# Kernel tuning notes

Hardware: AMD Instinct MI355X
Metric: run time of the kernel (lower is better)

## Reference

```python
import jax, jax.numpy as jnp
import numpy as np

B, Q, D, N = 128, 20, 11, 100000  # batch, produced vectors per sample, feature dim, song DB size
EPS = 1e-8  # torch cosine_similarity eps


def setup_inputs() -> dict:
    key = jax.random.key(0)
    ks = jax.random.split(key, 8)
    x = jax.random.normal(ks[0], (B, 5, 11), dtype=jnp.float32)
    W1 = jax.random.normal(ks[1], (55, 128), dtype=jnp.float32) * 0.1
    b1 = jnp.zeros((128,), dtype=jnp.float32)
    W2 = jax.random.normal(ks[2], (128, 64), dtype=jnp.float32) * 0.1
    b2 = jnp.zeros((64,), dtype=jnp.float32)
    W3 = jax.random.normal(ks[3], (64, Q * D), dtype=jnp.float32) * 0.1
    b3 = jnp.zeros((Q * D,), dtype=jnp.float32)
    songs = jax.random.normal(ks[4], (N, D), dtype=jnp.float32)
    return {"x": x, "W1": W1, "b1": b1, "W2": W2, "b2": b2, "W3": W3, "b3": b3, "songs": songs}


def reference(x, W1, b1, W2, b2, W3, b3, songs):
    # Encoder MLP: Flatten -> Linear -> ReLU -> Linear -> ReLU -> Linear
    h = x.reshape(x.shape[0], -1)                 # [B, 55]
    h = jax.nn.relu(h @ W1 + b1)                  # [B, 128]
    h = jax.nn.relu(h @ W2 + b2)                  # [B, 64]
    produced = (h @ W3 + b3).reshape(-1, Q, D)    # [B, 20, 11]

    # Batched cosine-similarity kNN (k=1 / argmax) against the song DB.
    # torch cosine_similarity: a.b / (max(||a||, eps) * max(||b||, eps))
    p_norm = produced / jnp.maximum(jnp.linalg.norm(produced, axis=-1, keepdims=True), EPS)
    s_norm = songs / jnp.maximum(jnp.linalg.norm(songs, axis=-1, keepdims=True), EPS)
    sim = jnp.einsum('bqd,nd->bqn', p_norm, s_norm)  # [B, Q, N]
    best = jnp.argmax(sim, axis=-1)                  # [B, Q]
    return songs[best]                                # [B, Q, D]
```

## Files before the change

kernel.cpp:

```cpp
#include <hip/hip_runtime.h>
#include <math.h>

#define EPS 1e-8f

constexpr int B_ = 128;
constexpr int Q_ = 20;
constexpr int D_ = 11;
constexpr int N_ = 100000;
constexpr int DP_ = 12;
constexpr int NPAIR = B_ * Q_;
constexpr int NCH = 2500;
constexpr int CS = N_ / NCH;
constexpr int NG = CS / 4;
constexpr int TPB = 128;
constexpr int PPT = 4;
constexpr int REP = NPAIR / (PPT * TPB);
constexpr int CPB = 2;
constexpr int NPB = NCH / CPB;
constexpr int MPAD = (NPB + 7) / 8;
constexpr int SGRID = 8 * MPAD * REP;

typedef __attribute__((ext_vector_type(4))) float f4;

__global__ void prep_kernel(const float* __restrict__ x,
                            const float* __restrict__ W1, const float* __restrict__ b1,
                            const float* __restrict__ W2, const float* __restrict__ b2,
                            const float* __restrict__ W3, const float* __restrict__ b3,
                            const float* __restrict__ songs,
                            float* __restrict__ pnorm, float* __restrict__ snorm,
                            int do_snorm)
{
    const int t = threadIdx.x;
    if (blockIdx.x >= B_) {
        if (!do_snorm) return;
        const int i = (blockIdx.x - B_) * blockDim.x + t;
        if (i >= N_) return;
        float v[DP_]; float ss = 0.0f;
#pragma unroll
        for (int d = 0; d < D_; ++d) { v[d] = songs[(size_t)i * D_ + d]; ss += v[d] * v[d]; }
        float nrm = fmaxf(sqrtf(ss), EPS);
#pragma unroll
        for (int d = 0; d < D_; ++d) v[d] /= nrm;
        v[D_] = 0.0f;
        float4* o = reinterpret_cast<float4*>(snorm + (size_t)i * DP_);
        o[0] = make_float4(v[0], v[1], v[2], v[3]);
        o[1] = make_float4(v[4], v[5], v[6], v[7]);
        o[2] = make_float4(v[8], v[9], v[10], v[11]);
        return;
    }
    __shared__ float xr[55];
    __shared__ float h1[128];
    __shared__ float h2[64];
    __shared__ float prod[220];
    const int b = blockIdx.x;
    if (t < 55) xr[t] = x[b * 55 + t];
    __syncthreads();
    if (t < 128) {
        float s = b1[t];
        for (int k = 0; k < 55; ++k) s += xr[k] * W1[k * 128 + t];
        h1[t] = fmaxf(s, 0.0f);
    }
    __syncthreads();
    if (t < 64) {
        float s = b2[t];
        for (int k = 0; k < 128; ++k) s += h1[k] * W2[k * 64 + t];
        h2[t] = fmaxf(s, 0.0f);
    }
    __syncthreads();
    if (t < 220) {
        float s = b3[t];
        for (int k = 0; k < 64; ++k) s += h2[k] * W3[k * 220 + t];
        prod[t] = s;
    }
    __syncthreads();
    if (t < Q_) {
        float ss = 0.0f;
        for (int d = 0; d < D_; ++d) { float v = prod[t * D_ + d]; ss += v * v; }
        float nrm = fmaxf(sqrtf(ss), EPS);
        float* o = pnorm + (b * Q_ + t) * DP_;
        for (int d = 0; d < D_; ++d) o[d] = prod[t * D_ + d] / nrm;
        o[D_] = 0.0f;
    }
}

__device__ __forceinline__ float dot11v(f4 qa, f4 qb, f4 qc,
                                        float4 a, float4 b, float4 c)
{
    float x = qa.x * a.x;
    x = fmaf(qa.y, a.y, x);
    x = fmaf(qa.z, a.z, x);
    x = fmaf(qa.w, a.w, x);
    x = fmaf(qb.x, b.x, x);
    x = fmaf(qb.y, b.y, x);
    x = fmaf(qb.z, b.z, x);
    x = fmaf(qb.w, b.w, x);
    x = fmaf(qc.x, c.x, x);
    x = fmaf(qc.y, c.y, x);
    x = fmaf(qc.z, c.z, x);
    return x;
}

__device__ __forceinline__ unsigned int fkey(float f)
{
    unsigned int b = __float_as_uint(f);
    return (b & 0x80000000u) ? ~b : (b | 0x80000000u);
}

__device__ __forceinline__ unsigned long long pack_vi(float v, int idx)
{
    return ((unsigned long long)fkey(v) << 32) | (unsigned long long)(0xFFFFFFFFu - (unsigned int)idx);
}

#define QLOAD(P, PTR) \
    asm volatile("global_load_dwordx4 %0, %3, off\n\t" \
                 "global_load_dwordx4 %1, %3, off offset:16\n\t" \
                 "global_load_dwordx4 %2, %3, off offset:32" \
                 : "=&v"(q##P##a), "=&v"(q##P##b), "=&v"(q##P##c) \
                 : "v"(PTR) : "memory")

#define QWAIT() \
    asm volatile("s_waitcnt vmcnt(0)" \
                 : "+v"(qAa), "+v"(qAb), "+v"(qAc), "+v"(qBa), "+v"(qBb), "+v"(qBc), \
                   "+v"(qCa), "+v"(qCb), "+v"(qCc), "+v"(qDa), "+v"(qDb), "+v"(qDc) \
                 :: "memory")

#define PMAXV(P, GCUR) { \
    float d0 = dot11v(q##P##a, q##P##b, q##P##c, s0, s1,  s2);  \
    float d1 = dot11v(q##P##a, q##P##b, q##P##c, s3, s4,  s5);  \
    float d2 = dot11v(q##P##a, q##P##b, q##P##c, s6, s7,  s8);  \
    float d3 = dot11v(q##P##a, q##P##b, q##P##c, s9, s10, s11); \
    float mx = fmaxf(fmaxf(d0, d1), fmaxf(d2, d3)); \
    if (mx > bv##P) { bv##P = mx; gi##P = (GCUR); } \
}

#define GSTEP(L4, GIDX, GOFF) { \
    const float4* vg = (L4) + (GIDX) * 12; \
    float4 s0 = vg[0], s1 = vg[1], s2  = vg[2],  s3  = vg[3],  s4  = vg[4],  s5  = vg[5]; \
    float4 s6 = vg[6], s7 = vg[7], s8  = vg[8],  s9  = vg[9],  s10 = vg[10], s11 = vg[11]; \
    PMAXV(A, (GOFF) + (GIDX)) PMAXV(B, (GOFF) + (GIDX)) \
    PMAXV(C, (GOFF) + (GIDX)) PMAXV(D, (GOFF) + (GIDX)) \
}

#define FINI(P, POFF) { \
    int gsel = gi##P; \
    int cs = (gsel >= NG) ? 1 : 0; \
    int gg = gsel - cs * NG; \
    const float4* vg = reinterpret_cast<const float4*>(lds[cs]) + gg * 12; \
    float4 s0 = vg[0], s1 = vg[1], s2  = vg[2],  s3  = vg[3],  s4  = vg[4],  s5  = vg[5]; \
    float4 s6 = vg[6], s7 = vg[7], s8  = vg[8],  s9  = vg[9],  s10 = vg[10], s11 = vg[11]; \
    float d0 = dot11v(q##P##a, q##P##b, q##P##c, s0, s1,  s2);  \
    float d1 = dot11v(q##P##a, q##P##b, q##P##c, s3, s4,  s5);  \
    float d2 = dot11v(q##P##a, q##P##b, q##P##c, s6, s7,  s8);  \
    float d3 = dot11v(q##P##a, q##P##b, q##P##c, s9, s10, s11); \
    int base = (c0 + cs) * CS + gg * 4; \
    int idx = base; \
    if (d3 == bv##P) idx = base + 3; \
    if (d2 == bv##P) idx = base + 2; \
    if (d1 == bv##P) idx = base + 1; \
    if (d0 == bv##P) idx = base; \
    atomicMax(&res[jb + (POFF) * TPB], pack_vi(bv##P, idx)); \
}

__global__ __launch_bounds__(TPB, 2)
void sim17_kernel(const float* __restrict__ pnorm,
                  const float* __restrict__ snorm,
                  unsigned long long* __restrict__ res)
{
    __shared__ __align__(16) float lds[CPB][CS * DP_];
    const int bid = blockIdx.x;
    const int u = bid & 7;
    const int kk = bid >> 3;
    const int r = kk % REP;
    const int m = kk / REP;
    const int cpair = u + 8 * m;
    if (cpair >= NPB) return;
    const int t = threadIdx.x;
    const int c0 = cpair * CPB;

    const float4* s40 = reinterpret_cast<const float4*>(snorm) + (size_t)c0 * CS * 3;
    const float4* s41 = s40 + CS * 3;
    float4* b0 = reinterpret_cast<float4*>(lds[0]);
    float4* b1 = reinterpret_cast<float4*>(lds[1]);

    if (t < CS * 3) b0[t] = s40[t];

    const int jb = r * (PPT * TPB) + t;
    f4 qAa, qAb, qAc, qBa, qBb, qBc, qCa, qCb, qCc, qDa, qDb, qDc;
    {
        const float* qp0 = pnorm + (size_t)(jb + 0 * TPB) * DP_;
        const float* qp1 = pnorm + (size_t)(jb + 1 * TPB) * DP_;
        const float* qp2 = pnorm + (size_t)(jb + 2 * TPB) * DP_;
        const float* qp3 = pnorm + (size_t)(jb + 3 * TPB) * DP_;
        QLOAD(A, qp0);
        QLOAD(B, qp1);
        QLOAD(C, qp2);
        QLOAD(D, qp3);
    }
    QWAIT();

    float4 r0 = make_float4(0.f, 0.f, 0.f, 0.f);
    if (t < CS * 3) r0 = s41[t];

    __syncthreads();

    float bvA = -1e30f, bvB = -1e30f, bvC = -1e30f, bvD = -1e30f;
    int giA = 0, giB = 0, giC = 0, giD = 0;

    for (int g = 0; g < NG; ++g) {
        GSTEP(b0, g, 0);
    }

    if (t < CS * 3) b1[t] = r0;
    __syncthreads();

    for (int g = 0; g < NG; ++g) {
        GSTEP(b1, g, NG);
    }

    FINI(A, 0) FINI(B, 1) FINI(C, 2) FINI(D, 3)
}

template<int FNCH>
__global__ void sim6f_kernel(const float* __restrict__ pnorm,
                             const float* __restrict__ songs,
                             unsigned long long* __restrict__ res)
{
    constexpr int FCS = N_ / FNCH;
    const int chunk = blockIdx.x;
    const int j = blockIdx.y * 256 + threadIdx.x;

    float qv[D_];
#pragma unroll
    for (int d = 0; d < D_; ++d) qv[d] = pnorm[j * DP_ + d];

    float bestv = -1e30f;
    int   besti = 0;
    const int base = chunk * FCS;
    for (int i = base; i < base + FCS; ++i) {
        float sv[D_]; float ss = 0.0f;
#pragma unroll
        for (int d = 0; d < D_; ++d) { sv[d] = songs[(size_t)i * D_ + d]; ss += sv[d] * sv[d]; }
        float nrm = fmaxf(sqrtf(ss), EPS);
        float a = qv[0] * (sv[0] / nrm);
#pragma unroll
        for (int d = 1; d < D_; ++d) a = fmaf(qv[d], sv[d] / nrm, a);
        if (a > bestv) { bestv = a; besti = i; }
    }
    atomicMax(&res[j], pack_vi(bestv, besti));
}

__global__ void gather_kernel(const unsigned long long* __restrict__ res,
                              const float* __restrict__ songs, float* __restrict__ out)
{
    const int j = blockIdx.x * blockDim.x + threadIdx.x;
    if (j >= NPAIR) return;
    const unsigned int idx = 0xFFFFFFFFu - (unsigned int)(res[j] & 0xFFFFFFFFull);
#pragma unroll
    for (int d = 0; d < D_; ++d) out[(size_t)j * D_ + d] = songs[(size_t)idx * D_ + d];
}

extern "C" void kernel_launch(void* const* d_in, const int* in_sizes, int n_in,
                              void* d_out, int out_size, void* d_ws, size_t ws_size,
                              hipStream_t stream)
{
    const float* x     = (const float*)d_in[0];
    const float* W1    = (const float*)d_in[1];
    const float* b1    = (const float*)d_in[2];
    const float* W2    = (const float*)d_in[3];
    const float* b2    = (const float*)d_in[4];
    const float* W3    = (const float*)d_in[5];
    const float* b3    = (const float*)d_in[6];
    const float* songs = (const float*)d_in[7];
    float* out = (float*)d_out;

    constexpr size_t PN = (size_t)NPAIR * DP_;
    constexpr size_t SN = (size_t)N_ * DP_;
    float* pnorm = (float*)d_ws;
    constexpr int SNB = (N_ + 255) / 256;

    const size_t need_full = (PN + SN) * sizeof(float) + (size_t)NPAIR * 8 + 64;
    const size_t need_min  = PN * sizeof(float) + (size_t)NPAIR * 8 + 64;

    if (ws_size >= need_full) {
        float* snorm = pnorm + PN;
        unsigned long long* res =
            (unsigned long long*)(((uintptr_t)(snorm + SN) + 7) & ~(uintptr_t)7);
        hipMemsetAsync(res, 0, (size_t)NPAIR * 8, stream);
        prep_kernel<<<B_ + SNB, 256, 0, stream>>>(x, W1, b1, W2, b2, W3, b3, songs,
                                                  pnorm, snorm, 1);
        sim17_kernel<<<SGRID, TPB, 0, stream>>>(pnorm, snorm, res);
        gather_kernel<<<(NPAIR + 255) / 256, 256, 0, stream>>>(res, songs, out);
    } else if (ws_size >= need_min) {
        unsigned long long* res =
            (unsigned long long*)(((uintptr_t)(pnorm + PN) + 7) & ~(uintptr_t)7);
        hipMemsetAsync(res, 0, (size_t)NPAIR * 8, stream);
        prep_kernel<<<B_, 256, 0, stream>>>(x, W1, b1, W2, b2, W3, b3, songs,
                                            pnorm, nullptr, 0);
        constexpr int FNCH = 250;
        sim6f_kernel<FNCH><<<dim3(FNCH, NPAIR / 256), 256, 0, stream>>>(pnorm, songs, res);
        gather_kernel<<<(NPAIR + 255) / 256, 256, 0, stream>>>(res, songs, out);
    }
}
```

Baseline: 95.37 us.

## Split song-vector reads between LDS and global loads with larger chunks

Chunk size grows from 40 to 100 songs per chunk (NCH 2500 to 1000), which cuts the grid size and the number of atomic merges. Only the first half of each 4-song group is staged in LDS. The second half is read directly from global memory (likely L1/L2 hits), so LDS bandwidth and footprint are shared with the vector memory path. The inner loops are unrolled by 2. This risks more global-load latency in the hot loop and fewer blocks for load balancing.

```diff
diff --git a/kernel.cpp b/kernel.cpp
--- a/kernel.cpp
+++ b/kernel.cpp
@@ -9,7 +9,7 @@
 constexpr int N_ = 100000;
 constexpr int DP_ = 12;
 constexpr int NPAIR = B_ * Q_;
-constexpr int NCH = 2500;
+constexpr int NCH = 1000;
 constexpr int CS = N_ / NCH;
 constexpr int NG = CS / 4;
 constexpr int TPB = 128;
@@ -19,6 +19,7 @@
 constexpr int NPB = NCH / CPB;
 constexpr int MPAD = (NPB + 7) / 8;
 constexpr int SGRID = 8 * MPAD * REP;
+constexpr int LHALF = NG * 6;
 
 typedef __attribute__((ext_vector_type(4))) float f4;
 
@@ -133,10 +134,11 @@
     if (mx > bv##P) { bv##P = mx; gi##P = (GCUR); } \
 }
 
-#define GSTEP(L4, GIDX, GOFF) { \
-    const float4* vg = (L4) + (GIDX) * 12; \
-    float4 s0 = vg[0], s1 = vg[1], s2  = vg[2],  s3  = vg[3],  s4  = vg[4],  s5  = vg[5]; \
-    float4 s6 = vg[6], s7 = vg[7], s8  = vg[8],  s9  = vg[9],  s10 = vg[10], s11 = vg[11]; \
+#define GSTEP(L4, GP, GIDX, GOFF) { \
+    const float4* vg = (L4) + (GIDX) * 6; \
+    float4 s0 = vg[0], s1 = vg[1], s2 = vg[2], s3 = vg[3], s4 = vg[4], s5 = vg[5]; \
+    const float4* wg = (GP) + (GIDX) * 12 + 6; \
+    float4 s6 = wg[0], s7 = wg[1], s8 = wg[2], s9 = wg[3], s10 = wg[4], s11 = wg[5]; \
     PMAXV(A, (GOFF) + (GIDX)) PMAXV(B, (GOFF) + (GIDX)) \
     PMAXV(C, (GOFF) + (GIDX)) PMAXV(D, (GOFF) + (GIDX)) \
 }
@@ -145,9 +147,10 @@
     int gsel = gi##P; \
     int cs = (gsel >= NG) ? 1 : 0; \
     int gg = gsel - cs * NG; \
-    const float4* vg = reinterpret_cast<const float4*>(lds[cs]) + gg * 12; \
-    float4 s0 = vg[0], s1 = vg[1], s2  = vg[2],  s3  = vg[3],  s4  = vg[4],  s5  = vg[5]; \
-    float4 s6 = vg[6], s7 = vg[7], s8  = vg[8],  s9  = vg[9],  s10 = vg[10], s11 = vg[11]; \
+    const float4* vg = reinterpret_cast<const float4*>(lds[cs]) + gg * 6; \
+    float4 s0 = vg[0], s1 = vg[1], s2 = vg[2], s3 = vg[3], s4 = vg[4], s5 = vg[5]; \
+    const float4* wg = s40 + (size_t)cs * CS * 3 + gg * 12 + 6; \
+    float4 s6 = wg[0], s7 = wg[1], s8 = wg[2], s9 = wg[3], s10 = wg[4], s11 = wg[5]; \
     float d0 = dot11v(q##P##a, q##P##b, q##P##c, s0, s1,  s2);  \
     float d1 = dot11v(q##P##a, q##P##b, q##P##c, s3, s4,  s5);  \
     float d2 = dot11v(q##P##a, q##P##b, q##P##c, s6, s7,  s8);  \
@@ -162,11 +165,11 @@
 }
 
 __global__ __launch_bounds__(TPB, 2)
-void sim17_kernel(const float* __restrict__ pnorm,
+void sim19_kernel(const float* __restrict__ pnorm,
                   const float* __restrict__ snorm,
                   unsigned long long* __restrict__ res)
 {
-    __shared__ __align__(16) float lds[CPB][CS * DP_];
+    __shared__ __align__(16) float lds[CPB][LHALF * 4];
     const int bid = blockIdx.x;
     const int u = bid & 7;
     const int kk = bid >> 3;
@@ -182,7 +185,15 @@
     float4* b0 = reinterpret_cast<float4*>(lds[0]);
     float4* b1 = reinterpret_cast<float4*>(lds[1]);
 
-    if (t < CS * 3) b0[t] = s40[t];
+    {
+        int g = t / 6, i = t - g * 6;
+        b0[t] = s40[g * 12 + i];
+        int f2 = t + TPB;
+        if (f2 < LHALF) {
+            int g2 = f2 / 6, i2 = f2 - g2 * 6;
+            b0[f2] = s40[g2 * 12 + i2];
+        }
+    }
 
     const int jb = r * (PPT * TPB) + t;
     f4 qAa, qAb, qAc, qBa, qBb, qBc, qCa, qCb, qCc, qDa, qDb, qDc;
@@ -198,23 +209,34 @@
     }
     QWAIT();
 
-    float4 r0 = make_float4(0.f, 0.f, 0.f, 0.f);
-    if (t < CS * 3) r0 = s41[t];
+    float4 r0, r1 = make_float4(0.f, 0.f, 0.f, 0.f);
+    {
+        int g = t / 6, i = t - g * 6;
+        r0 = s41[g * 12 + i];
+        int f2 = t + TPB;
+        if (f2 < LHALF) {
+            int g2 = f2 / 6, i2 = f2 - g2 * 6;
+            r1 = s41[g2 * 12 + i2];
+        }
+    }
 
     __syncthreads();
 
     float bvA = -1e30f, bvB = -1e30f, bvC = -1e30f, bvD = -1e30f;
     int giA = 0, giB = 0, giC = 0, giD = 0;
 
+#pragma unroll 2
     for (int g = 0; g < NG; ++g) {
-        GSTEP(b0, g, 0);
-    }
-
-    if (t < CS * 3) b1[t] = r0;
-    __syncthreads();
-
+        GSTEP(b0, s40, g, 0);
+    }
+
+    b1[t] = r0;
+    if (t + TPB < LHALF) b1[t + TPB] = r1;
+    __syncthreads();
+
+#pragma unroll 2
     for (int g = 0; g < NG; ++g) {
-        GSTEP(b1, g, NG);
+        GSTEP(b1, s41, g, NG);
     }
 
     FINI(A, 0) FINI(B, 1) FINI(C, 2) FINI(D, 3)
@@ -288,7 +310,7 @@
         hipMemsetAsync(res, 0, (size_t)NPAIR * 8, stream);
         prep_kernel<<<B_ + SNB, 256, 0, stream>>>(x, W1, b1, W2, b2, W3, b3, songs,
                                                   pnorm, snorm, 1);
-        sim17_kernel<<<SGRID, TPB, 0, stream>>>(pnorm, snorm, res);
+        sim19_kernel<<<SGRID, TPB, 0, stream>>>(pnorm, snorm, res);
         gather_kernel<<<(NPAIR + 255) / 256, 256, 0, stream>>>(res, songs, out);
     } else if (ws_size >= need_min) {
         unsigned long long* res =
```

Result: no change. 96.39 us (+1.1%).
